# Performance work log

Hardware: AMD Instinct MI355X
Metric: run time of the kernel (lower is better)

The kernel has to match this reference:

```python
import jax, jax.numpy as jnp
import numpy as np

D_MODEL = 128
N_HEADS = 4
D_K = D_V = 32
LN_EPS = 1e-5


def setup_inputs() -> dict:
    key = jax.random.key(0)
    ks = jax.random.split(key, 12)
    B, S = 8, 2048
    scale = 1.0 / np.sqrt(D_MODEL)
    inp = {
        "Q": jax.random.normal(ks[0], (B, S, D_MODEL), jnp.float32),
        "K": jax.random.normal(ks[1], (B, S, D_MODEL), jnp.float32),
        "V": jax.random.normal(ks[2], (B, S, D_MODEL), jnp.float32),
        "attn_mask": jnp.zeros((B, S, S), jnp.bool_),
        # learned params (torch Linear stored as [in, out] so y = x @ W + b)
        "wq": jax.random.normal(ks[3], (D_MODEL, N_HEADS * D_K), jnp.float32) * scale,
        "bq": jnp.zeros((N_HEADS * D_K,), jnp.float32),
        "wk": jax.random.normal(ks[4], (D_MODEL, N_HEADS * D_K), jnp.float32) * scale,
        "bk": jnp.zeros((N_HEADS * D_K,), jnp.float32),
        "wv": jax.random.normal(ks[5], (D_MODEL, N_HEADS * D_V), jnp.float32) * scale,
        "bv": jnp.zeros((N_HEADS * D_V,), jnp.float32),
        "wo": jax.random.normal(ks[6], (N_HEADS * D_V, D_MODEL), jnp.float32) * scale,
        "bo": jnp.zeros((D_MODEL,), jnp.float32),
        "gamma": jnp.ones((D_MODEL,), jnp.float32),
        "beta": jnp.zeros((D_MODEL,), jnp.float32),
    }
    return inp


def _layer_norm(x, gamma, beta):
    mu = jnp.mean(x, axis=-1, keepdims=True)
    var = jnp.mean(jnp.square(x - mu), axis=-1, keepdims=True)
    return (x - mu) * jax.lax.rsqrt(var + LN_EPS) * gamma + beta


def reference(Q, K, V, attn_mask, wq, bq, wk, bk, wv, bv, wo, bo, gamma, beta):
    B, S, _ = Q.shape
    residual = Q
    # project and split heads: [B, H, S, Dk]
    q = (Q @ wq + bq).reshape(B, S, N_HEADS, D_K).transpose(0, 2, 1, 3)
    k = (K @ wk + bk).reshape(B, S, N_HEADS, D_K).transpose(0, 2, 1, 3)
    v = (V @ wv + bv).reshape(B, S, N_HEADS, D_V).transpose(0, 2, 1, 3)
    scores = jnp.einsum("bhqd,bhkd->bhqk", q, k) / np.sqrt(D_K)
    scores = jnp.where(attn_mask[:, None, :, :], -1e9, scores)
    attn = jax.nn.softmax(scores, axis=-1)
    context = jnp.einsum("bhqk,bhkd->bhqd", attn, v)
    context = context.transpose(0, 2, 1, 3).reshape(B, S, N_HEADS * D_V)
    output = context @ wo + bo
    out = _layer_norm(output + residual, gamma, beta)
    return out, attn
```

## Files before the change

kernel.cpp:

```cpp
#include <hip/hip_runtime.h>

typedef _Float16 f16;
typedef __attribute__((ext_vector_type(8))) _Float16 f16x8;
typedef __attribute__((ext_vector_type(4))) _Float16 f16x4;
typedef __attribute__((ext_vector_type(4))) float f32x4;
typedef unsigned int u32;
typedef __attribute__((ext_vector_type(2))) unsigned int u32x2;
typedef __attribute__((ext_vector_type(4))) unsigned int u32x4;

#define S_LEN 2048
#define NB 8
#define NH 4
#define DM 128
#define DK 32

static __device__ __forceinline__ f32x4 mfma_16x16x32(f16x8 a, f16x8 b, f32x4 c) {
  return __builtin_amdgcn_mfma_f32_16x16x32_f16(a, b, c, 0, 0, 0);
}

__global__ __launch_bounds__(256) void pack_mask_kernel(
    const unsigned char* __restrict__ mask, u32* __restrict__ words)
{
  const int tid = blockIdx.x * 256 + threadIdx.x;
  u32x4 v = *(const u32x4*)(mask + (size_t)tid * 16);
  u32 bits = 0;
#pragma unroll
  for (int i = 0; i < 4; ++i) {
    u32 u = v[i];
#pragma unroll
    for (int k = 0; k < 4; ++k)
      bits |= (((u >> (8 * k)) & 0xffu) ? 1u : 0u) << (4 * i + k);
  }
  u32 other = __shfl_xor(bits, 1);
  if ((threadIdx.x & 1) == 0) words[tid >> 1] = bits | (other << 16);
}

__global__ __launch_bounds__(256) void proj_kernel(
    const float* __restrict__ Qx, const float* __restrict__ Kx, const float* __restrict__ Vx,
    const float* __restrict__ wq, const float* __restrict__ bq,
    const float* __restrict__ wk, const float* __restrict__ bk,
    const float* __restrict__ wv, const float* __restrict__ bv,
    f16* __restrict__ qh, f16* __restrict__ kh, f16* __restrict__ vt)
{
  const int mode = blockIdx.y;
  const float* X = (mode == 0) ? Qx : (mode == 1) ? Kx : Vx;
  const float* W = (mode == 0) ? wq : (mode == 1) ? wk : wv;
  const float* Bp = (mode == 0) ? bq : (mode == 1) ? bk : bv;

  __shared__ float xt[16][128];
  const int t = threadIdx.x;
  const int row0 = blockIdx.x * 16;

  const f32x4* src = (const f32x4*)(X + (size_t)row0 * DM);
  f32x4* dst4 = (f32x4*)(&xt[0][0]);
  dst4[t] = src[t];
  dst4[t + 256] = src[t + 256];
  __syncthreads();

  const int j = t & 127;
  const int rg = t >> 7;
  float acc[8];
#pragma unroll
  for (int r = 0; r < 8; ++r) acc[r] = 0.f;
  for (int k = 0; k < 128; ++k) {
    float wkj = W[k * 128 + j];
#pragma unroll
    for (int r = 0; r < 8; ++r) acc[r] += xt[rg * 8 + r][k] * wkj;
  }
  const float bb = Bp[j];
  const int hh = j >> 5, dd = j & 31;

  if (mode < 2) {
    const float scale = (mode == 0) ? 0.17677669529663687f : 1.0f;
    f16* outp = (mode == 0) ? qh : kh;
#pragma unroll
    for (int r = 0; r < 8; ++r) {
      int row = row0 + rg * 8 + r;
      int b = row >> 11, s = row & (S_LEN - 1);
      outp[((size_t)(b * NH + hh) * S_LEN + s) * DK + dd] = (f16)((acc[r] + bb) * scale);
    }
  } else {
    int b = row0 >> 11;
    int sA = (row0 & (S_LEN - 1)) + rg * 8;
    f16* base = vt + (size_t)(b * NH + hh) * DK * S_LEN;
    int t4 = sA >> 5;
    int u0 = sA & 31;
    int half = u0 >> 4;
    int hi4 = (u0 >> 2) & 3;
    f16* p = base + (size_t)t4 * 1024 + dd * 32 + half * 4;
    f16x4 lo, hi8;
#pragma unroll
    for (int r = 0; r < 4; ++r) lo[r] = (f16)(acc[r] + bb);
#pragma unroll
    for (int r = 0; r < 4; ++r) hi8[r] = (f16)(acc[r + 4] + bb);
    *(f16x4*)(p + hi4 * 8) = lo;
    *(f16x4*)(p + (hi4 + 1) * 8) = hi8;
  }
}

__global__ __launch_bounds__(256, 4) void attn_kernel(
    const f16* __restrict__ qh, const f16* __restrict__ kh, const f16* __restrict__ vt,
    const u32* __restrict__ words,
    float* __restrict__ attn, float* __restrict__ ctx)
{
  const int bx = blockIdx.x;
  const int bh = bx >> 6;
  const int qp = bx & 63;
  const int wave = threadIdx.x >> 6;
  const int tile = wave >> 1;
  const int half = wave & 1;
  const int lane = threadIdx.x & 63;
  const int ln = lane & 15, hi = lane >> 4;
  const int b = bh >> 2, h = bh & 3;
  const int qrow = qp * 32 + tile * 16 + ln;
  const int kv0 = half * (S_LEN / 2);

  __shared__ f32x4 ptile[4][16][16];
  __shared__ float sums[2][2][16];

  const f16* kbase = kh + (size_t)bh * S_LEN * DK;
  const f16* vbase = vt + (size_t)bh * DK * S_LEN;
  const u32* wrow = words + ((size_t)b * S_LEN + qrow) * (S_LEN / 32);

  const f16x8 qfrag = *(const f16x8*)(qh + ((size_t)bh * S_LEN + qrow) * DK + hi * 8);
  const f32x4 zero = {0.f, 0.f, 0.f, 0.f};

  float sum = 0.f;
  {
    const f16* kp = kbase + (size_t)(kv0 + ln) * DK + hi * 8;
    const u32* mp = wrow + (kv0 >> 5);
    f16x8 k0 = *(const f16x8*)(kp);
    f16x8 k1 = *(const f16x8*)(kp + 512);
    f16x8 k2 = *(const f16x8*)(kp + 1024);
    f16x8 k3 = *(const f16x8*)(kp + 1536);
    f16x8 k4 = *(const f16x8*)(kp + 2048);
    f16x8 k5 = *(const f16x8*)(kp + 2560);
    f16x8 k6 = *(const f16x8*)(kp + 3072);
    f16x8 k7 = *(const f16x8*)(kp + 3584);
    u32x4 mw = *(const u32x4*)mp;
    for (int it = 0; it < 8; ++it) {
      f16x8 n0, n1, n2, n3, n4, n5, n6, n7;
      u32x4 nm;
      if (it < 7) {
        n0 = *(const f16x8*)(kp + 4096);
        n1 = *(const f16x8*)(kp + 4608);
        n2 = *(const f16x8*)(kp + 5120);
        n3 = *(const f16x8*)(kp + 5632);
        n4 = *(const f16x8*)(kp + 6144);
        n5 = *(const f16x8*)(kp + 6656);
        n6 = *(const f16x8*)(kp + 7168);
        n7 = *(const f16x8*)(kp + 7680);
        nm = *(const u32x4*)(mp + 4);
      }
      f32x4 s0 = mfma_16x16x32(k0, qfrag, zero);
      f32x4 s1 = mfma_16x16x32(k1, qfrag, zero);
      f32x4 s2 = mfma_16x16x32(k2, qfrag, zero);
      f32x4 s3 = mfma_16x16x32(k3, qfrag, zero);
      f32x4 s4 = mfma_16x16x32(k4, qfrag, zero);
      f32x4 s5 = mfma_16x16x32(k5, qfrag, zero);
      f32x4 s6 = mfma_16x16x32(k6, qfrag, zero);
      f32x4 s7 = mfma_16x16x32(k7, qfrag, zero);
#pragma unroll
      for (int r = 0; r < 4; ++r) {
        float e0 = ((mw[0] >> (4 * hi + r)) & 1) ? 0.f : __expf(s0[r]);
        float e1 = ((mw[0] >> (16 + 4 * hi + r)) & 1) ? 0.f : __expf(s1[r]);
        float e2 = ((mw[1] >> (4 * hi + r)) & 1) ? 0.f : __expf(s2[r]);
        float e3 = ((mw[1] >> (16 + 4 * hi + r)) & 1) ? 0.f : __expf(s3[r]);
        float e4 = ((mw[2] >> (4 * hi + r)) & 1) ? 0.f : __expf(s4[r]);
        float e5 = ((mw[2] >> (16 + 4 * hi + r)) & 1) ? 0.f : __expf(s5[r]);
        float e6 = ((mw[3] >> (4 * hi + r)) & 1) ? 0.f : __expf(s6[r]);
        float e7 = ((mw[3] >> (16 + 4 * hi + r)) & 1) ? 0.f : __expf(s7[r]);
        sum += ((e0 + e1) + (e2 + e3)) + ((e4 + e5) + (e6 + e7));
      }
      k0 = n0; k1 = n1; k2 = n2; k3 = n3;
      k4 = n4; k5 = n5; k6 = n6; k7 = n7;
      mw = nm;
      kp += 4096;
      mp += 4;
    }
  }
  sum += __shfl_xor(sum, 16);
  sum += __shfl_xor(sum, 32);
  if (lane < 16) sums[tile][half][ln] = sum;
  __syncthreads();
  const float inv = 1.f / (sums[tile][0][ln] + sums[tile][1][ln]);

  f32x4 c0 = zero, c1 = zero;
  {
    const f16* kp = kbase + (size_t)(kv0 + ln) * DK + hi * 8;
    const f16* vp = vbase + (size_t)(kv0 >> 5) * 1024 + ln * 32 + hi * 8;
    const u32* mp = wrow + (kv0 >> 5);
    f16x8 k0 = *(const f16x8*)(kp);
    f16x8 k1 = *(const f16x8*)(kp + 512);
    f16x8 k2 = *(const f16x8*)(kp + 1024);
    f16x8 k3 = *(const f16x8*)(kp + 1536);
    u32x2 mw = *(const u32x2*)mp;
    for (int it = 0; it < 16; ++it) {
      const int kv = kv0 + it * 64;
      f16x8 v0 = *(const f16x8*)(vp);
      f16x8 v1 = *(const f16x8*)(vp + 512);
      f16x8 v2 = *(const f16x8*)(vp + 1024);
      f16x8 v3 = *(const f16x8*)(vp + 1536);
      f16x8 n0, n1, n2, n3;
      u32x2 nm;
      if (it < 15) {
        n0 = *(const f16x8*)(kp + 2048);
        n1 = *(const f16x8*)(kp + 2560);
        n2 = *(const f16x8*)(kp + 3072);
        n3 = *(const f16x8*)(kp + 3584);
        nm = *(const u32x2*)(mp + 2);
      }
      f32x4 s0 = mfma_16x16x32(k0, qfrag, zero);
      f32x4 s1 = mfma_16x16x32(k1, qfrag, zero);
      f32x4 p0, p1;
#pragma unroll
      for (int r = 0; r < 4; ++r) {
        p0[r] = ((mw[0] >> (4 * hi + r)) & 1) ? 0.f : __expf(s0[r]) * inv;
        p1[r] = ((mw[0] >> (16 + 4 * hi + r)) & 1) ? 0.f : __expf(s1[r]) * inv;
      }
      f16x8 pfA;
#pragma unroll
      for (int r = 0; r < 4; ++r) { pfA[r] = (f16)p0[r]; pfA[r + 4] = (f16)p1[r]; }
      c0 = mfma_16x16x32(v0, pfA, c0);
      c1 = mfma_16x16x32(v1, pfA, c1);
      ptile[wave][ln][(0 + hi) ^ (ln & 7)] = p0;
      ptile[wave][ln][(4 + hi) ^ (ln & 7)] = p1;
      f32x4 s2 = mfma_16x16x32(k2, qfrag, zero);
      f32x4 s3 = mfma_16x16x32(k3, qfrag, zero);
      f32x4 p2, p3;
#pragma unroll
      for (int r = 0; r < 4; ++r) {
        p2[r] = ((mw[1] >> (4 * hi + r)) & 1) ? 0.f : __expf(s2[r]) * inv;
        p3[r] = ((mw[1] >> (16 + 4 * hi + r)) & 1) ? 0.f : __expf(s3[r]) * inv;
      }
      f16x8 pfB;
#pragma unroll
      for (int r = 0; r < 4; ++r) { pfB[r] = (f16)p2[r]; pfB[r + 4] = (f16)p3[r]; }
      c0 = mfma_16x16x32(v2, pfB, c0);
      c1 = mfma_16x16x32(v3, pfB, c1);
      ptile[wave][ln][(8 + hi) ^ (ln & 7)] = p2;
      ptile[wave][ln][(12 + hi) ^ (ln & 7)] = p3;
#pragma unroll
      for (int s = 0; s < 4; ++s) {
        int row = s * 4 + hi;
        f32x4 val = ptile[wave][row][ln ^ (row & 7)];
        int qr = qp * 32 + tile * 16 + row;
        float* dst = attn + ((size_t)bh * S_LEN + qr) * S_LEN + kv + ln * 4;
        __builtin_nontemporal_store(val, (f32x4*)dst);
      }
      k0 = n0; k1 = n1; k2 = n2; k3 = n3;
      mw = nm;
      kp += 2048;
      vp += 2048;
      mp += 2;
    }
  }

  if (half == 1) {
    float* cb = (float*)&ptile[tile * 2 + 1][0][0];
#pragma unroll
    for (int r = 0; r < 4; ++r) {
      cb[ln * 32 + hi * 4 + r] = c0[r];
      cb[ln * 32 + 16 + hi * 4 + r] = c1[r];
    }
  }
  __syncthreads();
  if (half == 0) {
    const float* cb = (const float*)&ptile[tile * 2 + 1][0][0];
#pragma unroll
    for (int r = 0; r < 4; ++r) {
      c0[r] += cb[ln * 32 + hi * 4 + r];
      c1[r] += cb[ln * 32 + 16 + hi * 4 + r];
    }
    float* crow = ctx + ((size_t)b * S_LEN + qrow) * DM + h * DK;
    *(f32x4*)(crow + hi * 4) = c0;
    *(f32x4*)(crow + 16 + hi * 4) = c1;
  }
}

__global__ __launch_bounds__(256) void out_ln_kernel(
    const float* __restrict__ ctx, const float* __restrict__ Qin,
    const float* __restrict__ wo, const float* __restrict__ bo,
    const float* __restrict__ gamma, const float* __restrict__ beta,
    float* __restrict__ out)
{
  __shared__ float xt[16][128];
  __shared__ float yt[16][128];
  const int t = threadIdx.x;
  const int row0 = blockIdx.x * 16;

  const f32x4* src = (const f32x4*)(ctx + (size_t)row0 * DM);
  f32x4* dst4 = (f32x4*)(&xt[0][0]);
  dst4[t] = src[t];
  dst4[t + 256] = src[t + 256];
  __syncthreads();

  const int j = t & 127;
  const int rg = t >> 7;
  float acc[8];
#pragma unroll
  for (int r = 0; r < 8; ++r) acc[r] = 0.f;
  for (int k = 0; k < 128; ++k) {
    float wkj = wo[k * 128 + j];
#pragma unroll
    for (int r = 0; r < 8; ++r) acc[r] += xt[rg * 8 + r][k] * wkj;
  }
  const float bb = bo[j];
#pragma unroll
  for (int r = 0; r < 8; ++r) {
    int row = row0 + rg * 8 + r;
    yt[rg * 8 + r][j] = acc[r] + bb + Qin[(size_t)row * DM + j];
  }
  __syncthreads();

  const int wv = t >> 6, lnid = t & 63;
#pragma unroll
  for (int r = 0; r < 4; ++r) {
    int row = wv * 4 + r;
    float a = yt[row][lnid];
    float b2 = yt[row][lnid + 64];
    float s = a + b2, sq = a * a + b2 * b2;
#pragma unroll
    for (int off = 32; off >= 1; off >>= 1) {
      s += __shfl_xor(s, off);
      sq += __shfl_xor(sq, off);
    }
    float mu = s * (1.f / 128.f);
    float var = sq * (1.f / 128.f) - mu * mu;
    float rstd = rsqrtf(var + 1e-5f);
    size_t orow = (size_t)(row0 + row) * DM;
    out[orow + lnid] = (a - mu) * rstd * gamma[lnid] + beta[lnid];
    out[orow + lnid + 64] = (b2 - mu) * rstd * gamma[lnid + 64] + beta[lnid + 64];
  }
}

extern "C" void kernel_launch(void* const* d_in, const int* in_sizes, int n_in,
                              void* d_out, int out_size, void* d_ws, size_t ws_size,
                              hipStream_t stream) {
  const float* Q    = (const float*)d_in[0];
  const float* K    = (const float*)d_in[1];
  const float* V    = (const float*)d_in[2];
  const unsigned char* mask = (const unsigned char*)d_in[3];
  const float* wq   = (const float*)d_in[4];
  const float* bq   = (const float*)d_in[5];
  const float* wk   = (const float*)d_in[6];
  const float* bk   = (const float*)d_in[7];
  const float* wv   = (const float*)d_in[8];
  const float* bv   = (const float*)d_in[9];
  const float* wo   = (const float*)d_in[10];
  const float* bo   = (const float*)d_in[11];
  const float* gamma= (const float*)d_in[12];
  const float* beta = (const float*)d_in[13];

  const size_t HEAD_ELEMS = (size_t)NB * NH * S_LEN * DK;

  f16* qh = (f16*)d_ws;
  f16* kh = qh + HEAD_ELEMS;
  f16* vt = kh + HEAD_ELEMS;
  float* ctx = (float*)(vt + HEAD_ELEMS);
  u32* words = (u32*)(ctx + (size_t)NB * S_LEN * DM);

  float* out  = (float*)d_out;
  float* attn = out + (size_t)NB * S_LEN * DM;

  pack_mask_kernel<<<8192, 256, 0, stream>>>(mask, words);
  proj_kernel<<<dim3(1024, 3), 256, 0, stream>>>(Q, K, V, wq, bq, wk, bk, wv, bv, qh, kh, vt);
  attn_kernel<<<2048, 256, 0, stream>>>(qh, kh, vt, words, attn, ctx);
  out_ln_kernel<<<1024, 256, 0, stream>>>(ctx, Q, wo, bo, gamma, beta, out);
}
```

Measured before the change: 200.2 us.

## Use exp2 with folded log2e scale, log-sum normalization, mask fast path, double-buffered P tile

Folds log2(e) into the Q scale so softmax can use the native exp2 instruction, and replaces the per-element multiply by 1/sum with an additive -log2(sum) inside the exponent. Adds a wave-uniform fast path that skips the per-element mask tests when every mask word in the tile is zero. Converts probabilities to f16 with packed RTZ conversions and double-buffers the LDS probability tile, so the global store of the attention tile is deferred by one iteration and can overlap the next MFMA work. The exp-based normalization and RTZ conversion change rounding slightly.

```diff
diff --git a/kernel.cpp b/kernel.cpp
--- a/kernel.cpp
+++ b/kernel.cpp
@@ -3,6 +3,7 @@
 typedef _Float16 f16;
 typedef __attribute__((ext_vector_type(8))) _Float16 f16x8;
 typedef __attribute__((ext_vector_type(4))) _Float16 f16x4;
+typedef __attribute__((ext_vector_type(2))) __fp16 fp16x2;
 typedef __attribute__((ext_vector_type(4))) float f32x4;
 typedef unsigned int u32;
 typedef __attribute__((ext_vector_type(2))) unsigned int u32x2;
@@ -17,6 +18,11 @@
 static __device__ __forceinline__ f32x4 mfma_16x16x32(f16x8 a, f16x8 b, f32x4 c) {
   return __builtin_amdgcn_mfma_f32_16x16x32_f16(a, b, c, 0, 0, 0);
 }
+static __device__ __forceinline__ float exp2f_fast(float x) {
+  return __builtin_amdgcn_exp2f(x);
+}
+
+union H8 { f16x8 v; fp16x2 h[4]; };
 
 __global__ __launch_bounds__(256) void pack_mask_kernel(
     const unsigned char* __restrict__ mask, u32* __restrict__ words)
@@ -71,7 +77,7 @@
   const int hh = j >> 5, dd = j & 31;
 
   if (mode < 2) {
-    const float scale = (mode == 0) ? 0.17677669529663687f : 1.0f;
+    const float scale = (mode == 0) ? 0.25503531f : 1.0f;
     f16* outp = (mode == 0) ? qh : kh;
 #pragma unroll
     for (int r = 0; r < 8; ++r) {
@@ -115,7 +121,7 @@
   const int qrow = qp * 32 + tile * 16 + ln;
   const int kv0 = half * (S_LEN / 2);
 
-  __shared__ f32x4 ptile[4][16][16];
+  __shared__ f32x4 ptile[4][2][16][16];
   __shared__ float sums[2][2][16];
 
   const f16* kbase = kh + (size_t)bh * S_LEN * DK;
@@ -160,17 +166,33 @@
       f32x4 s5 = mfma_16x16x32(k5, qfrag, zero);
       f32x4 s6 = mfma_16x16x32(k6, qfrag, zero);
       f32x4 s7 = mfma_16x16x32(k7, qfrag, zero);
-#pragma unroll
-      for (int r = 0; r < 4; ++r) {
-        float e0 = ((mw[0] >> (4 * hi + r)) & 1) ? 0.f : __expf(s0[r]);
-        float e1 = ((mw[0] >> (16 + 4 * hi + r)) & 1) ? 0.f : __expf(s1[r]);
-        float e2 = ((mw[1] >> (4 * hi + r)) & 1) ? 0.f : __expf(s2[r]);
-        float e3 = ((mw[1] >> (16 + 4 * hi + r)) & 1) ? 0.f : __expf(s3[r]);
-        float e4 = ((mw[2] >> (4 * hi + r)) & 1) ? 0.f : __expf(s4[r]);
-        float e5 = ((mw[2] >> (16 + 4 * hi + r)) & 1) ? 0.f : __expf(s5[r]);
-        float e6 = ((mw[3] >> (4 * hi + r)) & 1) ? 0.f : __expf(s6[r]);
-        float e7 = ((mw[3] >> (16 + 4 * hi + r)) & 1) ? 0.f : __expf(s7[r]);
-        sum += ((e0 + e1) + (e2 + e3)) + ((e4 + e5) + (e6 + e7));
+      const u32 anyw = (mw[0] | mw[1]) | (mw[2] | mw[3]);
+      if (__any(anyw != 0u)) {
+#pragma unroll
+        for (int r = 0; r < 4; ++r) {
+          float e0 = ((mw[0] >> (4 * hi + r)) & 1) ? 0.f : exp2f_fast(s0[r]);
+          float e1 = ((mw[0] >> (16 + 4 * hi + r)) & 1) ? 0.f : exp2f_fast(s1[r]);
+          float e2 = ((mw[1] >> (4 * hi + r)) & 1) ? 0.f : exp2f_fast(s2[r]);
+          float e3 = ((mw[1] >> (16 + 4 * hi + r)) & 1) ? 0.f : exp2f_fast(s3[r]);
+          float e4 = ((mw[2] >> (4 * hi + r)) & 1) ? 0.f : exp2f_fast(s4[r]);
+          float e5 = ((mw[2] >> (16 + 4 * hi + r)) & 1) ? 0.f : exp2f_fast(s5[r]);
+          float e6 = ((mw[3] >> (4 * hi + r)) & 1) ? 0.f : exp2f_fast(s6[r]);
+          float e7 = ((mw[3] >> (16 + 4 * hi + r)) & 1) ? 0.f : exp2f_fast(s7[r]);
+          sum += ((e0 + e1) + (e2 + e3)) + ((e4 + e5) + (e6 + e7));
+        }
+      } else {
+#pragma unroll
+        for (int r = 0; r < 4; ++r) {
+          float e0 = exp2f_fast(s0[r]);
+          float e1 = exp2f_fast(s1[r]);
+          float e2 = exp2f_fast(s2[r]);
+          float e3 = exp2f_fast(s3[r]);
+          float e4 = exp2f_fast(s4[r]);
+          float e5 = exp2f_fast(s5[r]);
+          float e6 = exp2f_fast(s6[r]);
+          float e7 = exp2f_fast(s7[r]);
+          sum += ((e0 + e1) + (e2 + e3)) + ((e4 + e5) + (e6 + e7));
+        }
       }
       k0 = n0; k1 = n1; k2 = n2; k3 = n3;
       k4 = n4; k5 = n5; k6 = n6; k7 = n7;
@@ -183,7 +205,7 @@
   sum += __shfl_xor(sum, 32);
   if (lane < 16) sums[tile][half][ln] = sum;
   __syncthreads();
-  const float inv = 1.f / (sums[tile][0][ln] + sums[tile][1][ln]);
+  const float linv = -__builtin_amdgcn_logf(sums[tile][0][ln] + sums[tile][1][ln]);
 
   f32x4 c0 = zero, c1 = zero;
   {
@@ -195,6 +217,7 @@
     f16x8 k2 = *(const f16x8*)(kp + 1024);
     f16x8 k3 = *(const f16x8*)(kp + 1536);
     u32x2 mw = *(const u32x2*)mp;
+    int cb = 0;
     for (int it = 0; it < 16; ++it) {
       const int kv = kv0 + it * 64;
       f16x8 v0 = *(const f16x8*)(vp);
@@ -210,67 +233,99 @@
         n3 = *(const f16x8*)(kp + 3584);
         nm = *(const u32x2*)(mp + 2);
       }
+      if (it > 0) {
+#pragma unroll
+        for (int s = 0; s < 4; ++s) {
+          int row = s * 4 + hi;
+          f32x4 val = ptile[wave][cb ^ 1][row][ln ^ (row & 7)];
+          int qr = qp * 32 + tile * 16 + row;
+          float* dst = attn + ((size_t)bh * S_LEN + qr) * S_LEN + (kv - 64) + ln * 4;
+          __builtin_nontemporal_store(val, (f32x4*)dst);
+        }
+      }
       f32x4 s0 = mfma_16x16x32(k0, qfrag, zero);
       f32x4 s1 = mfma_16x16x32(k1, qfrag, zero);
       f32x4 p0, p1;
-#pragma unroll
-      for (int r = 0; r < 4; ++r) {
-        p0[r] = ((mw[0] >> (4 * hi + r)) & 1) ? 0.f : __expf(s0[r]) * inv;
-        p1[r] = ((mw[0] >> (16 + 4 * hi + r)) & 1) ? 0.f : __expf(s1[r]) * inv;
-      }
-      f16x8 pfA;
-#pragma unroll
-      for (int r = 0; r < 4; ++r) { pfA[r] = (f16)p0[r]; pfA[r + 4] = (f16)p1[r]; }
-      c0 = mfma_16x16x32(v0, pfA, c0);
-      c1 = mfma_16x16x32(v1, pfA, c1);
-      ptile[wave][ln][(0 + hi) ^ (ln & 7)] = p0;
-      ptile[wave][ln][(4 + hi) ^ (ln & 7)] = p1;
+      if (__any((mw[0] | mw[1]) != 0u)) {
+#pragma unroll
+        for (int r = 0; r < 4; ++r) {
+          p0[r] = ((mw[0] >> (4 * hi + r)) & 1) ? 0.f : exp2f_fast(s0[r] + linv);
+          p1[r] = ((mw[0] >> (16 + 4 * hi + r)) & 1) ? 0.f : exp2f_fast(s1[r] + linv);
+        }
+      } else {
+#pragma unroll
+        for (int r = 0; r < 4; ++r) {
+          p0[r] = exp2f_fast(s0[r] + linv);
+          p1[r] = exp2f_fast(s1[r] + linv);
+        }
+      }
+      H8 ua;
+      ua.h[0] = __builtin_amdgcn_cvt_pkrtz(p0[0], p0[1]);
+      ua.h[1] = __builtin_amdgcn_cvt_pkrtz(p0[2], p0[3]);
+      ua.h[2] = __builtin_amdgcn_cvt_pkrtz(p1[0], p1[1]);
+      ua.h[3] = __builtin_amdgcn_cvt_pkrtz(p1[2], p1[3]);
+      c0 = mfma_16x16x32(v0, ua.v, c0);
+      c1 = mfma_16x16x32(v1, ua.v, c1);
+      ptile[wave][cb][ln][(0 + hi) ^ (ln & 7)] = p0;
+      ptile[wave][cb][ln][(4 + hi) ^ (ln & 7)] = p1;
       f32x4 s2 = mfma_16x16x32(k2, qfrag, zero);
       f32x4 s3 = mfma_16x16x32(k3, qfrag, zero);
       f32x4 p2, p3;
-#pragma unroll
-      for (int r = 0; r < 4; ++r) {
-        p2[r] = ((mw[1] >> (4 * hi + r)) & 1) ? 0.f : __expf(s2[r]) * inv;
-        p3[r] = ((mw[1] >> (16 + 4 * hi + r)) & 1) ? 0.f : __expf(s3[r]) * inv;
-      }
-      f16x8 pfB;
-#pragma unroll
-      for (int r = 0; r < 4; ++r) { pfB[r] = (f16)p2[r]; pfB[r + 4] = (f16)p3[r]; }
-      c0 = mfma_16x16x32(v2, pfB, c0);
-      c1 = mfma_16x16x32(v3, pfB, c1);
-      ptile[wave][ln][(8 + hi) ^ (ln & 7)] = p2;
-      ptile[wave][ln][(12 + hi) ^ (ln & 7)] = p3;
-#pragma unroll
-      for (int s = 0; s < 4; ++s) {
-        int row = s * 4 + hi;
-        f32x4 val = ptile[wave][row][ln ^ (row & 7)];
-        int qr = qp * 32 + tile * 16 + row;
-        float* dst = attn + ((size_t)bh * S_LEN + qr) * S_LEN + kv + ln * 4;
-        __builtin_nontemporal_store(val, (f32x4*)dst);
-      }
+      if (__any(mw[1] != 0u)) {
+#pragma unroll
+        for (int r = 0; r < 4; ++r) {
+          p2[r] = ((mw[1] >> (4 * hi + r)) & 1) ? 0.f : exp2f_fast(s2[r] + linv);
+          p3[r] = ((mw[1] >> (16 + 4 * hi + r)) & 1) ? 0.f : exp2f_fast(s3[r] + linv);
+        }
+      } else {
+#pragma unroll
+        for (int r = 0; r < 4; ++r) {
+          p2[r] = exp2f_fast(s2[r] + linv);
+          p3[r] = exp2f_fast(s3[r] + linv);
+        }
+      }
+      H8 ub;
+      ub.h[0] = __builtin_amdgcn_cvt_pkrtz(p2[0], p2[1]);
+      ub.h[1] = __builtin_amdgcn_cvt_pkrtz(p2[2], p2[3]);
+      ub.h[2] = __builtin_amdgcn_cvt_pkrtz(p3[0], p3[1]);
+      ub.h[3] = __builtin_amdgcn_cvt_pkrtz(p3[2], p3[3]);
+      c0 = mfma_16x16x32(v2, ub.v, c0);
+      c1 = mfma_16x16x32(v3, ub.v, c1);
+      ptile[wave][cb][ln][(8 + hi) ^ (ln & 7)] = p2;
+      ptile[wave][cb][ln][(12 + hi) ^ (ln & 7)] = p3;
+
       k0 = n0; k1 = n1; k2 = n2; k3 = n3;
       mw = nm;
       kp += 2048;
       vp += 2048;
       mp += 2;
+      cb ^= 1;
+    }
+#pragma unroll
+    for (int s = 0; s < 4; ++s) {
+      int row = s * 4 + hi;
+      f32x4 val = ptile[wave][cb ^ 1][row][ln ^ (row & 7)];
+      int qr = qp * 32 + tile * 16 + row;
+      float* dst = attn + ((size_t)bh * S_LEN + qr) * S_LEN + (kv0 + 960) + ln * 4;
+      __builtin_nontemporal_store(val, (f32x4*)dst);
     }
   }
 
   if (half == 1) {
-    float* cb = (float*)&ptile[tile * 2 + 1][0][0];
+    float* cb2 = (float*)&ptile[tile * 2 + 1][0][0][0];
 #pragma unroll
     for (int r = 0; r < 4; ++r) {
-      cb[ln * 32 + hi * 4 + r] = c0[r];
-      cb[ln * 32 + 16 + hi * 4 + r] = c1[r];
+      cb2[ln * 32 + hi * 4 + r] = c0[r];
+      cb2[ln * 32 + 16 + hi * 4 + r] = c1[r];
     }
   }
   __syncthreads();
   if (half == 0) {
-    const float* cb = (const float*)&ptile[tile * 2 + 1][0][0];
+    const float* cb2 = (const float*)&ptile[tile * 2 + 1][0][0][0];
 #pragma unroll
     for (int r = 0; r < 4; ++r) {
-      c0[r] += cb[ln * 32 + hi * 4 + r];
-      c1[r] += cb[ln * 32 + 16 + hi * 4 + r];
+      c0[r] += cb2[ln * 32 + hi * 4 + r];
+      c1[r] += cb2[ln * 32 + 16 + hi * 4 + r];
     }
     float* crow = ctx + ((size_t)b * S_LEN + qrow) * DM + h * DK;
     *(f32x4*)(crow + hi * 4) = c0;
```

Result: slower. 205.0 us (+2.4%).
